# Optimization experiments

Measured on AMD Instinct MI355X. Metric: run time of the kernel, lower is better.

The kernel has to match this reference:

```python
import jax, jax.numpy as jnp
import numpy as np


def setup_inputs() -> dict:
    key = jax.random.key(0)
    x = jax.random.normal(key, (32, 8192, 64), dtype=jnp.float32)
    return {"x": x}


def reference(x) -> jnp.ndarray:
    # x: [B, N, D]
    B, N, D = x.shape
    mean = jnp.mean(x, axis=1, keepdims=True)          # [B, 1, D]
    xc = x - mean                                      # [B, N, D]
    # Centered third-order moment: mean over N of triple outer product.
    # Contract over N directly instead of materializing [B, N, D, D, D].
    third = jnp.einsum('bnd,bne,bnf->bdef', xc, xc, xc) / N  # [B, D, D, D]
    return third.reshape(B, -1)                        # [B, D^3]
```

## Files before the change

kernel.cpp:

```cpp
#include <hip/hip_runtime.h>
#include <stdint.h>

#define B_SZ 32
#define N_SZ 8192
#define D_SZ 64

typedef _Float16 half8 __attribute__((ext_vector_type(8)));
typedef float f32x4 __attribute__((ext_vector_type(4)));

#define AS1 __attribute__((address_space(1)))
#define AS3 __attribute__((address_space(3)))

#define MFMA16(Aop, Bop, Cop) __builtin_amdgcn_mfma_f32_16x16x32_f16(Aop, Bop, Cop, 0, 0, 0)


__global__ __launch_bounds__(256) void tp_mean_kernel(const float* __restrict__ x,
                                                      float* __restrict__ sums) {
    const int b    = blockIdx.x >> 5;
    const int slab = blockIdx.x & 31;
    const int d4   = threadIdx.x & 15;
    const int nr   = threadIdx.x >> 4;
    const float* base = x + (size_t)b * (N_SZ * D_SZ) + (size_t)(slab * 256 + nr) * D_SZ + d4 * 4;
    f32x4 s = {0.f, 0.f, 0.f, 0.f};
#pragma unroll
    for (int i = 0; i < 16; i++)
        s += *(const f32x4*)(base + i * 16 * D_SZ);
    __shared__ f32x4 red[16][16];
    red[nr][d4] = s;
    __syncthreads();
    if (threadIdx.x < 16) {
        f32x4 tot = red[0][threadIdx.x];
#pragma unroll
        for (int j = 1; j < 16; j++) tot += red[j][threadIdx.x];
        atomicAdd(&sums[b * 64 + threadIdx.x * 4 + 0], tot[0]);
        atomicAdd(&sums[b * 64 + threadIdx.x * 4 + 1], tot[1]);
        atomicAdd(&sums[b * 64 + threadIdx.x * 4 + 2], tot[2]);
        atomicAdd(&sums[b * 64 + threadIdx.x * 4 + 3], tot[3]);
    }
}

__global__ __launch_bounds__(256) void tp_transpose_kernel(const float* __restrict__ x,
                                                           const float* __restrict__ sums,
                                                           _Float16* __restrict__ xcS) {
    const int b    = blockIdx.x >> 6;
    const int tp   = blockIdx.x & 63;
    const int t    = threadIdx.x;
    const int tile = tp * 2 + (t >> 7);
    const int r8   = (t >> 4) & 7;
    const int dq   = t & 15;

    f32x4 mean4 = *(const f32x4*)(sums + b * 64 + dq * 4) * (1.0f / (float)N_SZ);
    const float* src = x + (size_t)b * (N_SZ * D_SZ) + (size_t)(tile * 64 + r8 * 8) * D_SZ + dq * 4;
    f32x4 v[8];
#pragma unroll
    for (int i = 0; i < 8; i++)
        v[i] = *(const f32x4*)(src + i * D_SZ);

    _Float16* dstb = xcS + (size_t)b * (N_SZ * D_SZ) + (size_t)tile * 4096;
#pragma unroll
    for (int c = 0; c < 4; c++) {
        const int d   = dq * 4 + c;
        const int ccp = r8 ^ (d & 7);
        half8 o;
#pragma unroll
        for (int i = 0; i < 8; i++)
            o[i] = (_Float16)(v[i][c] - mean4[c]);
        *(half8*)(dstb + d * 64 + ccp * 8) = o;
    }
}

__global__ __launch_bounds__(256, 2) void tp_gemm_kernel(const _Float16* __restrict__ xcS,
                                                         float* __restrict__ out) {
    const int b    = blockIdx.x;
    const int eg   = blockIdx.y;
    const int tid  = threadIdx.x;
    const int lane = tid & 63;
    const int wv   = tid >> 6;
    const int h    = wv & 1;
    const int p    = wv >> 1;
    const int q    = lane >> 4;
    const int m    = lane & 15;
    const int e0   = eg * 4 + p * 2;

    __shared__ __align__(16) char ldsraw[65536];
    float* redL = (float*)ldsraw;

    const _Float16* gbase = xcS + (size_t)b * (N_SZ * D_SZ)
                          + (size_t)h * (N_SZ / 2) * D_SZ
                          + (size_t)(p * 2048 + lane * 8);

    int aOff[2][4], sOff[2][2];
#pragma unroll
    for (int ks = 0; ks < 2; ks++) {
        const int c = ks * 4 + q;
#pragma unroll
        for (int i = 0; i < 4; i++) {
            const int r = i * 16 + m;
            aOff[ks][i] = r * 128 + ((c ^ (r & 7)) * 16);
        }
#pragma unroll
        for (int j = 0; j < 2; j++) {
            const int e = e0 + j;
            sOff[ks][j] = e * 128 + ((c ^ (e & 7)) * 16);
        }
    }

    f32x4 acc[2][10];
#pragma unroll
    for (int ej = 0; ej < 2; ej++)
#pragma unroll
        for (int k = 0; k < 10; k++)
            acc[ej][k] = (f32x4){0.f, 0.f, 0.f, 0.f};

    auto stage = [&](int T, int bi) {
        _Float16* lb = (_Float16*)(ldsraw + bi * 32768 + h * 16384 + p * 4096);
        const _Float16* gb = gbase + (size_t)T * 8192;
#pragma unroll
        for (int g = 0; g < 2; g++)
#pragma unroll
            for (int k = 0; k < 4; k++)
                __builtin_amdgcn_global_load_lds(
                    (const AS1 void*)(gb + g * 4096 + k * 512),
                    (AS3 void*)(lb + g * 4096 + k * 512), 16, 0, 0);
    };

    stage(0, 0);

    for (int T = 0; T < 32; T++) {
        __syncthreads();
        if (T < 31) stage(T + 1, (T + 1) & 1);
        const char* hb = ldsraw + (T & 1) * 32768 + h * 16384;
#pragma unroll
        for (int g = 0; g < 2; g++) {
            const char* tb = hb + g * 8192;
#pragma unroll
            for (int ks = 0; ks < 2; ks++) {
                half8 A0 = *(const half8*)(tb + aOff[ks][0]);
                half8 A1 = *(const half8*)(tb + aOff[ks][1]);
                half8 A2 = *(const half8*)(tb + aOff[ks][2]);
                half8 A3 = *(const half8*)(tb + aOff[ks][3]);
                half8 S0 = *(const half8*)(tb + sOff[ks][0]);
                half8 S1 = *(const half8*)(tb + sOff[ks][1]);
#pragma unroll
                for (int ej = 0; ej < 2; ej++) {
                    half8 S = ej ? S1 : S0;
                    half8 P0 = A0 * S;
                    half8 P1 = A1 * S;
                    half8 P2 = A2 * S;
                    half8 P3 = A3 * S;
                    acc[ej][0] = MFMA16(P0, A0, acc[ej][0]);
                    acc[ej][1] = MFMA16(P0, A1, acc[ej][1]);
                    acc[ej][2] = MFMA16(P0, A2, acc[ej][2]);
                    acc[ej][3] = MFMA16(P0, A3, acc[ej][3]);
                    acc[ej][4] = MFMA16(P1, A1, acc[ej][4]);
                    acc[ej][5] = MFMA16(P1, A2, acc[ej][5]);
                    acc[ej][6] = MFMA16(P1, A3, acc[ej][6]);
                    acc[ej][7] = MFMA16(P2, A2, acc[ej][7]);
                    acc[ej][8] = MFMA16(P2, A3, acc[ej][8]);
                    acc[ej][9] = MFMA16(P3, A3, acc[ej][9]);
                }
            }
        }
    }
    __syncthreads();

    const int rbase = p * 5120 + lane * 4;
    if (h == 1) {
#pragma unroll
        for (int ej = 0; ej < 2; ej++)
#pragma unroll
            for (int k = 0; k < 10; k++)
                *(f32x4*)(redL + rbase + (ej * 10 + k) * 256) = acc[ej][k];
    }
    __syncthreads();
    if (h == 0) {
#pragma unroll
        for (int ej = 0; ej < 2; ej++)
#pragma unroll
            for (int k = 0; k < 10; k++)
                acc[ej][k] += *(const f32x4*)(redL + rbase + (ej * 10 + k) * 256);

        const float invn = 1.0f / (float)N_SZ;
        float* outb = out + (size_t)b * (D_SZ * D_SZ * D_SZ);
#pragma unroll
        for (int ej = 0; ej < 2; ej++) {
            const int e = e0 + ej;
            int idx = 0;
#pragma unroll
            for (int i = 0; i < 4; i++) {
#pragma unroll
                for (int j = i; j < 4; j++, idx++) {
                    f32x4 vsc = acc[ej][idx] * invn;
#pragma unroll
                    for (int r = 0; r < 4; r++)
                        outb[(size_t)(16 * i + q * 4 + r) * 4096 + e * 64 + 16 * j + m] = vsc[r];
                    if (i != j) {
                        *(f32x4*)&outb[(size_t)(16 * j + m) * 4096 + e * 64 + 16 * i + q * 4] = vsc;
                    }
                }
            }
        }
    }
}

extern "C" void kernel_launch(void* const* d_in, const int* in_sizes, int n_in,
                              void* d_out, int out_size, void* d_ws, size_t ws_size,
                              hipStream_t stream) {
    const float* x = (const float*)d_in[0];
    float* out = (float*)d_out;

    float* sums = (float*)d_ws;
    _Float16* xcS = (_Float16*)((char*)d_ws + 8192);

    hipMemsetAsync(sums, 0, B_SZ * D_SZ * sizeof(float), stream);
    tp_mean_kernel<<<dim3(B_SZ * 32), 256, 0, stream>>>(x, sums);
    tp_transpose_kernel<<<dim3(B_SZ * 64), 256, 0, stream>>>(x, sums, xcS);
    tp_gemm_kernel<<<dim3(32, 16), 256, 0, stream>>>(xcS, out);
}
```

Before: 182.1 us.

## Give each wave a private N-quarter and four e-slices, drop block barriers

The GEMM kernel's work split changes. Before, the four waves were split as two N-halves by two e-pairs. Now each wave takes its own quarter of N and computes all four e values of the block, so it reuses each A fragment across more MFMAs. Because each wave stages and reads only its own LDS slice, the per-iteration __syncthreads is replaced by explicit s_waitcnt on LDS and vector-memory counters. The trade-off is a 4-way, two-phase LDS reduction at the end and double the accumulator registers. The runtime-indexed accumulator selection in the store path also risks scratch spills.

```diff
diff --git a/kernel.cpp b/kernel.cpp
--- a/kernel.cpp
+++ b/kernel.cpp
@@ -75,116 +75,138 @@
     const int eg   = blockIdx.y;
     const int tid  = threadIdx.x;
     const int lane = tid & 63;
-    const int wv   = tid >> 6;
-    const int h    = wv & 1;
-    const int p    = wv >> 1;
+    const int h    = tid >> 6;
     const int q    = lane >> 4;
     const int m    = lane & 15;
-    const int e0   = eg * 4 + p * 2;
+    const int e0   = eg * 4;
 
     __shared__ __align__(16) char ldsraw[65536];
     float* redL = (float*)ldsraw;
 
     const _Float16* gbase = xcS + (size_t)b * (N_SZ * D_SZ)
-                          + (size_t)h * (N_SZ / 2) * D_SZ
-                          + (size_t)(p * 2048 + lane * 8);
-
-    int aOff[2][4], sOff[2][2];
-#pragma unroll
-    for (int ks = 0; ks < 2; ks++) {
-        const int c = ks * 4 + q;
-#pragma unroll
-        for (int i = 0; i < 4; i++) {
-            const int r = i * 16 + m;
-            aOff[ks][i] = r * 128 + ((c ^ (r & 7)) * 16);
-        }
-#pragma unroll
-        for (int j = 0; j < 2; j++) {
-            const int e = e0 + j;
-            sOff[ks][j] = e * 128 + ((c ^ (e & 7)) * 16);
-        }
-    }
-
-    f32x4 acc[2][10];
-#pragma unroll
-    for (int ej = 0; ej < 2; ej++)
+                          + (size_t)h * (N_SZ / 4) * D_SZ
+                          + (size_t)(lane * 8);
+
+    int aOff[4], sOff[4];
+#pragma unroll
+    for (int i = 0; i < 4; i++) {
+        const int r = i * 16 + m;
+        aOff[i] = r * 128 + ((q ^ (r & 7)) * 16);
+    }
+#pragma unroll
+    for (int j = 0; j < 4; j++) {
+        const int e = e0 + j;
+        sOff[j] = e * 128 + ((q ^ (e & 7)) * 16);
+    }
+
+    f32x4 acc[4][10];
+#pragma unroll
+    for (int ej = 0; ej < 4; ej++)
 #pragma unroll
         for (int k = 0; k < 10; k++)
             acc[ej][k] = (f32x4){0.f, 0.f, 0.f, 0.f};
 
     auto stage = [&](int T, int bi) {
-        _Float16* lb = (_Float16*)(ldsraw + bi * 32768 + h * 16384 + p * 4096);
-        const _Float16* gb = gbase + (size_t)T * 8192;
-#pragma unroll
-        for (int g = 0; g < 2; g++)
-#pragma unroll
-            for (int k = 0; k < 4; k++)
-                __builtin_amdgcn_global_load_lds(
-                    (const AS1 void*)(gb + g * 4096 + k * 512),
-                    (AS3 void*)(lb + g * 4096 + k * 512), 16, 0, 0);
+        _Float16* lb = (_Float16*)(ldsraw + bi * 32768 + h * 8192);
+        const _Float16* gb = gbase + (size_t)T * 4096;
+#pragma unroll
+        for (int k = 0; k < 8; k++)
+            __builtin_amdgcn_global_load_lds(
+                (const AS1 void*)(gb + k * 512),
+                (AS3 void*)(lb + k * 512), 16, 0, 0);
     };
 
     stage(0, 0);
 
     for (int T = 0; T < 32; T++) {
-        __syncthreads();
-        if (T < 31) stage(T + 1, (T + 1) & 1);
-        const char* hb = ldsraw + (T & 1) * 32768 + h * 16384;
-#pragma unroll
-        for (int g = 0; g < 2; g++) {
-            const char* tb = hb + g * 8192;
-#pragma unroll
-            for (int ks = 0; ks < 2; ks++) {
-                half8 A0 = *(const half8*)(tb + aOff[ks][0]);
-                half8 A1 = *(const half8*)(tb + aOff[ks][1]);
-                half8 A2 = *(const half8*)(tb + aOff[ks][2]);
-                half8 A3 = *(const half8*)(tb + aOff[ks][3]);
-                half8 S0 = *(const half8*)(tb + sOff[ks][0]);
-                half8 S1 = *(const half8*)(tb + sOff[ks][1]);
-#pragma unroll
-                for (int ej = 0; ej < 2; ej++) {
-                    half8 S = ej ? S1 : S0;
-                    half8 P0 = A0 * S;
-                    half8 P1 = A1 * S;
-                    half8 P2 = A2 * S;
-                    half8 P3 = A3 * S;
-                    acc[ej][0] = MFMA16(P0, A0, acc[ej][0]);
-                    acc[ej][1] = MFMA16(P0, A1, acc[ej][1]);
-                    acc[ej][2] = MFMA16(P0, A2, acc[ej][2]);
-                    acc[ej][3] = MFMA16(P0, A3, acc[ej][3]);
-                    acc[ej][4] = MFMA16(P1, A1, acc[ej][4]);
-                    acc[ej][5] = MFMA16(P1, A2, acc[ej][5]);
-                    acc[ej][6] = MFMA16(P1, A3, acc[ej][6]);
-                    acc[ej][7] = MFMA16(P2, A2, acc[ej][7]);
-                    acc[ej][8] = MFMA16(P2, A3, acc[ej][8]);
-                    acc[ej][9] = MFMA16(P3, A3, acc[ej][9]);
-                }
-            }
+        if (T < 31) {
+            asm volatile("s_waitcnt lgkmcnt(0)" ::: "memory");
+            stage(T + 1, (T + 1) & 1);
+            asm volatile("s_waitcnt vmcnt(8)" ::: "memory");
+        } else {
+            asm volatile("s_waitcnt vmcnt(0)" ::: "memory");
         }
-    }
-    __syncthreads();
-
-    const int rbase = p * 5120 + lane * 4;
+        const char* tb = ldsraw + (T & 1) * 32768 + h * 8192;
+#pragma unroll
+        for (int ks = 0; ks < 2; ks++) {
+            const int kx = ks << 6;
+            half8 A0 = *(const half8*)(tb + (aOff[0] ^ kx));
+            half8 A1 = *(const half8*)(tb + (aOff[1] ^ kx));
+            half8 A2 = *(const half8*)(tb + (aOff[2] ^ kx));
+            half8 A3 = *(const half8*)(tb + (aOff[3] ^ kx));
+#pragma unroll
+            for (int ej = 0; ej < 4; ej++) {
+                half8 S  = *(const half8*)(tb + (sOff[ej] ^ kx));
+                half8 P0 = A0 * S;
+                half8 P1 = A1 * S;
+                half8 P2 = A2 * S;
+                half8 P3 = A3 * S;
+                acc[ej][0] = MFMA16(P0, A0, acc[ej][0]);
+                acc[ej][1] = MFMA16(P0, A1, acc[ej][1]);
+                acc[ej][2] = MFMA16(P0, A2, acc[ej][2]);
+                acc[ej][3] = MFMA16(P0, A3, acc[ej][3]);
+                acc[ej][4] = MFMA16(P1, A1, acc[ej][4]);
+                acc[ej][5] = MFMA16(P1, A2, acc[ej][5]);
+                acc[ej][6] = MFMA16(P1, A3, acc[ej][6]);
+                acc[ej][7] = MFMA16(P2, A2, acc[ej][7]);
+                acc[ej][8] = MFMA16(P2, A3, acc[ej][8]);
+                acc[ej][9] = MFMA16(P3, A3, acc[ej][9]);
+            }
+        }
+    }
+
+    __syncthreads();
+    const int rb = lane * 4;
+    if (h != 0) {
+        float* dst = redL + (size_t)(h - 1) * 5120 + rb;
+#pragma unroll
+        for (int ej = 0; ej < 2; ej++)
+#pragma unroll
+            for (int k = 0; k < 10; k++)
+                *(f32x4*)(dst + (ej * 10 + k) * 256) = acc[ej][k];
+    }
+    __syncthreads();
+    if (h == 0) {
+#pragma unroll
+        for (int ej = 0; ej < 2; ej++)
+#pragma unroll
+            for (int k = 0; k < 10; k++) {
+                const float* s0 = redL + (ej * 10 + k) * 256 + rb;
+                acc[ej][k] += *(const f32x4*)(s0);
+                acc[ej][k] += *(const f32x4*)(s0 + 5120);
+                acc[ej][k] += *(const f32x4*)(s0 + 10240);
+            }
+    }
+    __syncthreads();
+    if (h != 1) {
+        const int region = (h == 0) ? 0 : (h - 1);
+        float* dst = redL + (size_t)region * 5120 + rb;
+#pragma unroll
+        for (int ej = 0; ej < 2; ej++)
+#pragma unroll
+            for (int k = 0; k < 10; k++)
+                *(f32x4*)(dst + (ej * 10 + k) * 256) = acc[2 + ej][k];
+    }
+    __syncthreads();
     if (h == 1) {
 #pragma unroll
         for (int ej = 0; ej < 2; ej++)
 #pragma unroll
-            for (int k = 0; k < 10; k++)
-                *(f32x4*)(redL + rbase + (ej * 10 + k) * 256) = acc[ej][k];
-    }
-    __syncthreads();
-    if (h == 0) {
-#pragma unroll
-        for (int ej = 0; ej < 2; ej++)
-#pragma unroll
-            for (int k = 0; k < 10; k++)
-                acc[ej][k] += *(const f32x4*)(redL + rbase + (ej * 10 + k) * 256);
-
+            for (int k = 0; k < 10; k++) {
+                const float* s0 = redL + (ej * 10 + k) * 256 + rb;
+                acc[2 + ej][k] += *(const f32x4*)(s0);
+                acc[2 + ej][k] += *(const f32x4*)(s0 + 5120);
+                acc[2 + ej][k] += *(const f32x4*)(s0 + 10240);
+            }
+    }
+
+    if (h < 2) {
         const float invn = 1.0f / (float)N_SZ;
         float* outb = out + (size_t)b * (D_SZ * D_SZ * D_SZ);
 #pragma unroll
-        for (int ej = 0; ej < 2; ej++) {
-            const int e = e0 + ej;
+        for (int ejL = 0; ejL < 2; ejL++) {
+            const int ej = h * 2 + ejL;
+            const int e  = e0 + ej;
             int idx = 0;
 #pragma unroll
             for (int i = 0; i < 4; i++) {
```

Measured after the change: 224.1 us. +23.1%, slower.
